# Kernel optimization log

Hardware: AMD Instinct MI355X
Metric: run time of the kernel (lower is better)

Reference implementation:

```python
import jax, jax.numpy as jnp
import numpy as np
from jax import lax

K = 31            # lcn_kernel_size
PAD = K // 2      # 15, 'same' padding
EPS = 1e-5
STRENGTH = 0.8    # CLAHE builds LCN with strength=0.8


def _box_filter(x):
    """31x31 uniform box filter (mean), implemented separably.

    Mathematically identical to conv2d with a (K,K) kernel of 1/K^2,
    padding K//2 (the torch module's mean_kernel conv).
    x: (B, 1, H, W)
    """
    kh = jnp.full((1, 1, K, 1), 1.0 / K, dtype=x.dtype)
    kw = jnp.full((1, 1, 1, K), 1.0 / K, dtype=x.dtype)
    dn = ('NCHW', 'OIHW', 'NCHW')
    y = lax.conv_general_dilated(x, kh, (1, 1), [(PAD, PAD), (0, 0)],
                                 dimension_numbers=dn)
    y = lax.conv_general_dilated(y, kw, (1, 1), [(0, 0), (PAD, PAD)],
                                 dimension_numbers=dn)
    return y


def setup_inputs() -> dict:
    key = jax.random.key(0)
    x = jax.random.uniform(key, (32, 1, 1024, 1024), dtype=jnp.float32)
    return {"x": x}


def reference(x):
    local_mean = _box_filter(x)
    local_sq_mean = _box_filter(x * x)
    local_var = local_sq_mean - local_mean * local_mean
    local_std = jnp.sqrt(jnp.maximum(local_var, EPS))
    normalized = (x - local_mean) / (local_std + EPS)
    enhanced = jax.nn.sigmoid(normalized * 0.5)
    return x * (1.0 - STRENGTH) + enhanced * STRENGTH
```

## Files before the change

### kernel.cpp

```cpp
#include <hip/hip_runtime.h>
#include <math.h>

#define HH 1024
#define WW 1024
#define PADK 15
#define RB 16
#define TPB 512
#define EPSV 1e-5f
#define INV_K2 (1.0f / 961.0f)

typedef float v4f __attribute__((ext_vector_type(4)));

__device__ __forceinline__ v4f ld4v(const float* p) {
    return *reinterpret_cast<const v4f*>(p);
}

__device__ __forceinline__ int swz4(int w) {
    return w ^ (((w >> 5) & 1) << 2);
}

__device__ __forceinline__ void hwin31(const float* __restrict__ sw, int bw,
                                       float wins[8]) {
    v4f R0 = ld4v(sw + swz4(bw));
    v4f R1 = ld4v(sw + swz4(bw + 4));
    v4f acc = R1;
    acc += ld4v(sw + swz4(bw + 8));
    acc += ld4v(sw + swz4(bw + 12));
    acc += ld4v(sw + swz4(bw + 16));
    acc += ld4v(sw + swz4(bw + 20));
    acc += ld4v(sw + swz4(bw + 24));
    acc += ld4v(sw + swz4(bw + 28));
    v4f R8 = ld4v(sw + swz4(bw + 32));
    v4f R9 = ld4v(sw + swz4(bw + 36));

    float base = (acc.x + acc.y) + (acc.z + acc.w);

    wins[0] = base + ((R0.y + R0.z) + R0.w);
    wins[1] = wins[0] + (R8.x - R0.y);
    wins[2] = wins[1] + (R8.y - R0.z);
    wins[3] = wins[2] + (R8.z - R0.w);
    wins[4] = wins[3] + (R8.w - R1.x);
    wins[5] = wins[4] + (R9.x - R1.y);
    wins[6] = wins[5] + (R9.y - R1.z);
    wins[7] = wins[6] + (R9.z - R1.w);
}

__global__ __launch_bounds__(TPB) void lcn_kernel(const float* __restrict__ x,
                                                  float* __restrict__ out) {
    __shared__ __align__(16) float sxl[8][552];
    __shared__ __align__(16) float sql[8][552];

    const int bid  = blockIdx.x;
    const int xcd  = bid & 7;
    const int k    = bid >> 3;
    const int b    = xcd * 4 + (k >> 4);
    const int seg  = k & 15;
    const int t    = threadIdx.x;
    const int w    = t >> 6;
    const int l    = t & 63;
    const int half = w & 1;
    const int band = w >> 1;
    const int r0   = seg * 64 + band * RB;
    const int wc0  = half * 512;
    const int c0   = wc0 + l * 8;
    const int bw   = 8 * l;

    float* __restrict__ sxw = sxl[w];
    float* __restrict__ sqw = sql[w];

    int hcol = 0;
    const bool hlane = (l < 8);
    if (l < 4)      hcol = wc0 - 16 + 4 * l;
    else if (l < 8) hcol = wc0 + 512 + 4 * (l - 4);
    const bool hvalid = hlane && (hcol >= 0) && (hcol < WW);
    const int  hw_    = (l < 4) ? 4 * l : 528 + 4 * (l - 4);
    const int  hidx   = swz4(hw_);

    const int ow0 = swz4(16 + 8 * l);
    const int ow1 = swz4(20 + 8 * l);

    const float* __restrict__ img  = x   + (size_t)b * HH * WW;
    float* __restrict__       oimg = out + (size_t)b * HH * WW;

    v4f sa  = {0.f, 0.f, 0.f, 0.f};
    v4f sb  = {0.f, 0.f, 0.f, 0.f};
    v4f qa  = {0.f, 0.f, 0.f, 0.f};
    v4f qb  = {0.f, 0.f, 0.f, 0.f};
    v4f hs  = {0.f, 0.f, 0.f, 0.f};
    v4f hs2 = {0.f, 0.f, 0.f, 0.f};

    {
        int lo = r0 - PADK; if (lo < 0) lo = 0;
        int hi = r0 + PADK; if (hi > HH - 1) hi = HH - 1;
        for (int r = lo; r <= hi; ++r) {
            const float* rowp = img + (size_t)r * WW;
            v4f va = ld4v(rowp + c0);
            v4f vb = ld4v(rowp + c0 + 4);
            sa += va;      sb += vb;
            qa += va * va; qb += vb * vb;
            if (hvalid) {
                v4f hv = ld4v(rowp + hcol);
                hs  += hv;
                hs2 += hv * hv;
            }
        }
    }

    for (int i = 0; i < RB; ++i) {
        const int orow = r0 + i;
        if (i > 0) {
            const int radd = orow + PADK;
            const int rsub = orow - PADK - 1;
            if (radd < HH) {
                const float* rowp = img + (size_t)radd * WW;
                v4f va = ld4v(rowp + c0);
                v4f vb = ld4v(rowp + c0 + 4);
                sa += va;      sb += vb;
                qa += va * va; qb += vb * vb;
                if (hvalid) {
                    v4f hv = ld4v(rowp + hcol);
                    hs  += hv;
                    hs2 += hv * hv;
                }
            }
            if (rsub >= 0) {
                const float* rowp = img + (size_t)rsub * WW;
                v4f va = ld4v(rowp + c0);
                v4f vb = ld4v(rowp + c0 + 4);
                sa -= va;      sb -= vb;
                qa -= va * va; qb -= vb * vb;
                if (hvalid) {
                    v4f hv = ld4v(rowp + hcol);
                    hs  -= hv;
                    hs2 -= hv * hv;
                }
            }
        }

        *reinterpret_cast<v4f*>(sxw + ow0) = sa;
        *reinterpret_cast<v4f*>(sxw + ow1) = sb;
        *reinterpret_cast<v4f*>(sqw + ow0) = qa;
        *reinterpret_cast<v4f*>(sqw + ow1) = qb;
        if (hlane) {
            *reinterpret_cast<v4f*>(sxw + hidx) = hs;
            *reinterpret_cast<v4f*>(sqw + hidx) = hs2;
        }

        const float* crow = img + (size_t)orow * WW + c0;
        const v4f xc0 = ld4v(crow);
        const v4f xc1 = ld4v(crow + 4);

        float winx[8], winq[8];
        hwin31(sxw, bw, winx);
        hwin31(sqw, bw, winq);

        v4f wxv0 = {winx[0], winx[1], winx[2], winx[3]};
        v4f wxv1 = {winx[4], winx[5], winx[6], winx[7]};
        v4f wqv0 = {winq[0], winq[1], winq[2], winq[3]};
        v4f wqv1 = {winq[4], winq[5], winq[6], winq[7]};
        v4f mean0 = wxv0 * INV_K2;
        v4f mean1 = wxv1 * INV_K2;
        v4f sqv0  = wqv0 * INV_K2;
        v4f sqv1  = wqv1 * INV_K2;
        v4f var0  = sqv0 - mean0 * mean0;
        v4f var1  = sqv1 - mean1 * mean1;
        const v4f epsv = {EPSV, EPSV, EPSV, EPSV};
        var0 = __builtin_elementwise_max(var0, epsv);
        var1 = __builtin_elementwise_max(var1, epsv);
        v4f d0 = xc0 - mean0;
        v4f d1 = xc1 - mean1;

        v4f o0, o1;
        #pragma unroll
        for (int q = 0; q < 4; ++q) {
            float rs  = __builtin_amdgcn_rsqf(var0[q]);
            float nrm = d0[q] * rs;
            float e   = __expf(-0.5f * nrm);
            o0[q] = xc0[q] * 0.2f + 0.8f * __builtin_amdgcn_rcpf(1.0f + e);
        }
        #pragma unroll
        for (int q = 0; q < 4; ++q) {
            float rs  = __builtin_amdgcn_rsqf(var1[q]);
            float nrm = d1[q] * rs;
            float e   = __expf(-0.5f * nrm);
            o1[q] = xc1[q] * 0.2f + 0.8f * __builtin_amdgcn_rcpf(1.0f + e);
        }
        float* orow_p = oimg + (size_t)orow * WW + c0;
        *reinterpret_cast<v4f*>(orow_p)     = o0;
        *reinterpret_cast<v4f*>(orow_p + 4) = o1;
    }
}

extern "C" void kernel_launch(void* const* d_in, const int* in_sizes, int n_in,
                              void* d_out, int out_size, void* d_ws, size_t ws_size,
                              hipStream_t stream) {
    const float* xin = (const float*)d_in[0];
    float* out = (float*)d_out;
    const int B = in_sizes[0] / (HH * WW);
    dim3 grid(B * 16);
    dim3 block(TPB);
    hipLaunchKernelGGL(lcn_kernel, grid, block, 0, stream, xin, out);
}
```

Before: 87.65 us.

## Split each band between two waves by row parity, doubling grid size

Each block now covers one column half of a 64-row segment, and the grid doubles. The two waves that shared a band now split its rows by parity: each handles 8 interleaved rows and advances its running column sums by two rows per step. The aim is more blocks and waves in flight to hide memory latency and balance load across CUs. In exchange each wave pays its own 31-row prime, so global reads for the prime and per-step adds roughly double.

```diff
diff --git a/kernel.cpp b/kernel.cpp
--- a/kernel.cpp
+++ b/kernel.cpp
@@ -4,7 +4,6 @@
 #define HH 1024
 #define WW 1024
 #define PADK 15
-#define RB 16
 #define TPB 512
 #define EPSV 1e-5f
 #define INV_K2 (1.0f / 961.0f)
@@ -45,6 +44,38 @@
     wins[7] = wins[6] + (R9.z - R1.w);
 }
 
+__device__ __forceinline__ void add_row(const float* __restrict__ img, int r,
+                                        int c0, int hcol, bool hvalid,
+                                        v4f& sa, v4f& sb, v4f& qa, v4f& qb,
+                                        v4f& hs, v4f& hs2) {
+    const float* rowp = img + (size_t)r * WW;
+    v4f va = ld4v(rowp + c0);
+    v4f vb = ld4v(rowp + c0 + 4);
+    sa += va;      sb += vb;
+    qa += va * va; qb += vb * vb;
+    if (hvalid) {
+        v4f hv = ld4v(rowp + hcol);
+        hs  += hv;
+        hs2 += hv * hv;
+    }
+}
+
+__device__ __forceinline__ void sub_row(const float* __restrict__ img, int r,
+                                        int c0, int hcol, bool hvalid,
+                                        v4f& sa, v4f& sb, v4f& qa, v4f& qb,
+                                        v4f& hs, v4f& hs2) {
+    const float* rowp = img + (size_t)r * WW;
+    v4f va = ld4v(rowp + c0);
+    v4f vb = ld4v(rowp + c0 + 4);
+    sa -= va;      sb -= vb;
+    qa -= va * va; qb -= vb * vb;
+    if (hvalid) {
+        v4f hv = ld4v(rowp + hcol);
+        hs  -= hv;
+        hs2 -= hv * hv;
+    }
+}
+
 __global__ __launch_bounds__(TPB) void lcn_kernel(const float* __restrict__ x,
                                                   float* __restrict__ out) {
     __shared__ __align__(16) float sxl[8][552];
@@ -53,14 +84,17 @@
     const int bid  = blockIdx.x;
     const int xcd  = bid & 7;
     const int k    = bid >> 3;
-    const int b    = xcd * 4 + (k >> 4);
-    const int seg  = k & 15;
+    const int b    = xcd * 4 + (k >> 5);
+    const int rem  = k & 31;
+    const int seg  = rem >> 1;
+    const int half = rem & 1;
     const int t    = threadIdx.x;
     const int w    = t >> 6;
     const int l    = t & 63;
-    const int half = w & 1;
     const int band = w >> 1;
-    const int r0   = seg * 64 + band * RB;
+    const int par  = w & 1;
+    const int r0   = seg * 64 + band * 16;
+    const int p0   = r0 + par;
     const int wc0  = half * 512;
     const int c0   = wc0 + l * 8;
     const int bw   = 8 * l;
@@ -90,51 +124,24 @@
     v4f hs2 = {0.f, 0.f, 0.f, 0.f};
 
     {
-        int lo = r0 - PADK; if (lo < 0) lo = 0;
-        int hi = r0 + PADK; if (hi > HH - 1) hi = HH - 1;
+        int lo = p0 - PADK; if (lo < 0) lo = 0;
+        int hi = p0 + PADK; if (hi > HH - 1) hi = HH - 1;
         for (int r = lo; r <= hi; ++r) {
-            const float* rowp = img + (size_t)r * WW;
-            v4f va = ld4v(rowp + c0);
-            v4f vb = ld4v(rowp + c0 + 4);
-            sa += va;      sb += vb;
-            qa += va * va; qb += vb * vb;
-            if (hvalid) {
-                v4f hv = ld4v(rowp + hcol);
-                hs  += hv;
-                hs2 += hv * hv;
-            }
-        }
-    }
-
-    for (int i = 0; i < RB; ++i) {
-        const int orow = r0 + i;
-        if (i > 0) {
-            const int radd = orow + PADK;
-            const int rsub = orow - PADK - 1;
-            if (radd < HH) {
-                const float* rowp = img + (size_t)radd * WW;
-                v4f va = ld4v(rowp + c0);
-                v4f vb = ld4v(rowp + c0 + 4);
-                sa += va;      sb += vb;
-                qa += va * va; qb += vb * vb;
-                if (hvalid) {
-                    v4f hv = ld4v(rowp + hcol);
-                    hs  += hv;
-                    hs2 += hv * hv;
-                }
-            }
-            if (rsub >= 0) {
-                const float* rowp = img + (size_t)rsub * WW;
-                v4f va = ld4v(rowp + c0);
-                v4f vb = ld4v(rowp + c0 + 4);
-                sa -= va;      sb -= vb;
-                qa -= va * va; qb -= vb * vb;
-                if (hvalid) {
-                    v4f hv = ld4v(rowp + hcol);
-                    hs  -= hv;
-                    hs2 -= hv * hv;
-                }
-            }
+            add_row(img, r, c0, hcol, hvalid, sa, sb, qa, qb, hs, hs2);
+        }
+    }
+
+    for (int j = 0; j < 8; ++j) {
+        const int orow = p0 + 2 * j;
+        if (j > 0) {
+            const int ra1 = orow + PADK - 1;
+            const int ra2 = orow + PADK;
+            const int rs1 = orow - PADK - 2;
+            const int rs2 = orow - PADK - 1;
+            if (ra1 < HH) add_row(img, ra1, c0, hcol, hvalid, sa, sb, qa, qb, hs, hs2);
+            if (ra2 < HH) add_row(img, ra2, c0, hcol, hvalid, sa, sb, qa, qb, hs, hs2);
+            if (rs1 >= 0) sub_row(img, rs1, c0, hcol, hvalid, sa, sb, qa, qb, hs, hs2);
+            if (rs2 >= 0) sub_row(img, rs2, c0, hcol, hvalid, sa, sb, qa, qb, hs, hs2);
         }
 
         *reinterpret_cast<v4f*>(sxw + ow0) = sa;
@@ -197,7 +204,7 @@
     const float* xin = (const float*)d_in[0];
     float* out = (float*)d_out;
     const int B = in_sizes[0] / (HH * WW);
-    dim3 grid(B * 16);
+    dim3 grid(B * 32);
     dim3 block(TPB);
     hipLaunchKernelGGL(lcn_kernel, grid, block, 0, stream, xin, out);
 }
```

Measured after the change: 88.85 us. Within noise of the previous version (+1.4%).
